# Kernel optimization log

Measured on AMD Instinct MI355X. Metric: run time of the kernel, lower is better.

Reference implementation:

```python
import jax, jax.numpy as jnp
import numpy as np

PE_SIZE = 16          # sqrt(num_patches=256)
HIDDEN_STRIDE = 2
CUBIC_A = -0.75       # torch bicubic coefficient


def cubic_resize_matrix(in_size, out_size, a=CUBIC_A):
    """(out_size, in_size) weights for torch bicubic, align_corners=False."""
    dst = np.arange(out_size)
    src = (dst + 0.5) * in_size / out_size - 0.5
    x0 = np.floor(src).astype(np.int64)
    W = np.zeros((out_size, in_size), np.float32)
    for k in range(-1, 3):  # 4 taps
        idx = np.clip(x0 + k, 0, in_size - 1)  # border replicate
        d = np.abs(src - (x0 + k))
        w = np.where(d <= 1.0, (a + 2) * d**3 - (a + 3) * d**2 + 1.0,
            np.where(d < 2.0, a * d**3 - 5 * a * d**2 + 8 * a * d - 4 * a, 0.0))
        np.add.at(W, (dst, idx), w.astype(np.float32))
    return W


def setup_inputs() -> dict:
    key = jax.random.key(0)
    k1, k2, k3, k4 = jax.random.split(key, 4)
    n_img, t, h, w = 8, 1, 64, 64
    total = n_img * t * h * w  # 32768 patches
    in_feat, d = 3 * 14 * 14, 1152
    return {
        "pixel_values": jax.random.normal(k1, (total, in_feat), jnp.float32),
        "w_patch": jax.random.normal(k2, (d, in_feat), jnp.float32) * 0.02,
        "b_patch": jax.random.normal(k3, (d,), jnp.float32) * 0.02,
        "pos_table": jax.random.normal(k4, (PE_SIZE * PE_SIZE, d), jnp.float32) * 0.02,
        "grid_thws": jnp.array([[t, h, w]] * n_img, jnp.int64),
    }


def _pos_embed(pos_table, grid):
    """grid: np int array (n_img, 3) -> (sum t*h*w, d) positional embeddings."""
    d = pos_table.shape[-1]
    pe_grid = pos_table.reshape(PE_SIZE, PE_SIZE, d)  # (H, W, d)
    s = HIDDEN_STRIDE
    pieces = []
    for t, h, w in grid:
        Wh = jnp.asarray(cubic_resize_matrix(PE_SIZE, int(h)))
        Ww = jnp.asarray(cubic_resize_matrix(PE_SIZE, int(w)))
        pe = jnp.einsum('hH,wW,HWd->hwd', Wh, Ww, pe_grid)  # (h, w, d)
        # hidden_stride window rearrange: (h,w,d) -> (h/s, w/s, s, s, d)
        pe = pe.reshape(h // s, s, w // s, s, d).transpose(0, 2, 1, 3, 4)
        pe = pe.reshape(h * w, d)
        pe = jnp.tile(pe, (int(t), 1))  # repeat over temporal dim
        pieces.append(pe)
    return jnp.concatenate(pieces, axis=0)


def reference(pixel_values, w_patch, b_patch, pos_table, grid_thws):
    # patch embedding (Linear)
    patch_embeds = pixel_values @ w_patch.T + b_patch  # (N, d)
    grid = np.asarray(grid_thws)  # static shapes per image
    pos = _pos_embed(pos_table, grid)
    return patch_embeds + pos
```

## Files before the change

### kernel.cpp

```cpp
#include <hip/hip_runtime.h>

typedef unsigned short ushort_t;
typedef unsigned int uint_t;

typedef __bf16 bf16x8 __attribute__((ext_vector_type(8)));
typedef float f32x4 __attribute__((ext_vector_type(4)));

#define KK 588
#define KP 608
#define NN 1152
#define MM 32768
#define POSROWS 4096
#define NSTEP 19
#define GRID 2304
#define CHUNKS_PER_ROW 76
#define BCHUNKS (NN * CHUNKS_PER_ROW)
#define BBLOCKS ((BCHUNKS + 255) / 256)


__device__ __forceinline__ void cubic_taps(int dst, float* w, int* idx) {
    const float A = -0.75f;
    float src = (float)dst * 0.25f - 0.25f;
    int x0 = (int)floorf(src);
    #pragma unroll
    for (int k = -1; k <= 2; ++k) {
        int i = x0 + k;
        int ic = i < 0 ? 0 : (i > 15 ? 15 : i);
        float d = fabsf(src - (float)i);
        float wt;
        if (d <= 1.0f)      wt = ((A + 2.0f) * d - (A + 3.0f)) * d * d + 1.0f;
        else if (d < 2.0f)  wt = ((A * d - 5.0f * A) * d + 8.0f * A) * d - 4.0f * A;
        else                wt = 0.0f;
        w[k + 1] = wt;
        idx[k + 1] = ic;
    }
}


__global__ void prep_kernel(const float* __restrict__ wp, ushort_t* __restrict__ wb,
                            const float* __restrict__ pt, const float* __restrict__ bias,
                            float* __restrict__ pos) {
    int b = blockIdx.x;
    if (b < BBLOCKS) {
        int c = b * 256 + threadIdx.x;
        if (c >= BCHUNKS) return;
        int row = c / CHUNKS_PER_ROW;
        int k0 = (c - row * CHUNKS_PER_ROW) * 8;
        const float* g = wp + (size_t)row * KK + k0;
        bf16x8 v;
        if (k0 + 8 <= KK) {
            f32x4 a = *(const f32x4*)g;
            f32x4 bb = *(const f32x4*)(g + 4);
            #pragma unroll
            for (int e = 0; e < 4; ++e) { v[e] = (__bf16)a[e]; v[e + 4] = (__bf16)bb[e]; }
        } else {
            #pragma unroll
            for (int e = 0; e < 8; ++e)
                v[e] = (k0 + e < KK) ? (__bf16)g[e] : (__bf16)0.f;
        }
        *(bf16x8*)(wb + (size_t)row * KP + k0) = v;
    } else {
        int n = b - BBLOCKS;
        int h = ((n >> 7) << 1) | ((n >> 1) & 1);
        int w = (((n >> 2) & 31) << 1) | (n & 1);
        float wh[4], ww[4];
        int ih[4], iw[4];
        cubic_taps(h, wh, ih);
        cubic_taps(w, ww, iw);
        const f32x4* pt4 = (const f32x4*)pt;
        const f32x4* bias4 = (const f32x4*)bias;
        for (int j = threadIdx.x; j < NN / 4; j += blockDim.x) {
            f32x4 s = bias4[j];
            #pragma unroll
            for (int a = 0; a < 4; ++a) {
                #pragma unroll
                for (int bq = 0; bq < 4; ++bq) {
                    float wt = wh[a] * ww[bq];
                    f32x4 vv = pt4[(ih[a] * 16 + iw[bq]) * (NN / 4) + j];
                    s.x += wt * vv.x; s.y += wt * vv.y; s.z += wt * vv.z; s.w += wt * vv.w;
                }
            }
            ((f32x4*)pos)[(size_t)n * (NN / 4) + j] = s;
        }
    }
}


__global__ __launch_bounds__(256, 3)
void gemm_kernel(const float* __restrict__ A,
                 const ushort_t* __restrict__ Bbf,
                 const float* __restrict__ pos,
                 float* __restrict__ out) {
    __shared__ __align__(16) ushort_t lA[2][128 * 32];
    __shared__ __align__(16) ushort_t lB[3][128 * 32];

    const int t = threadIdx.x;
    const int lane = t & 63;
    const int lm = lane & 15;
    const int lq = lane >> 4;
    const int wid = t >> 6;
    const int wm = wid >> 1, wn = wid & 1;

    const int arow = t >> 1;
    const int akh = (t & 1) * 16;
    const int asw = (arow >> 1) & 3;
    const int aq0 = (t & 1) * 2;

    int linear = (int)blockIdx.x;
    int xcd = linear & 7;
    int local = linear >> 3;
    int wg = xcd * (GRID / 8) + local;
    int mt = wg / 9;
    int nt = wg - mt * 9;
    const int bm = mt * 128;
    const int bn = nt * 128;

    f32x4 acc[4][4] = {};
    f32x4 rA0[4], rA1[4];

    auto loadA_fast = [&](int ks, f32x4* r) {
        const float* g = A + (size_t)(bm + arow) * KK + ks * 32 + akh;
        r[0] = *(const f32x4*)g;
        r[1] = *(const f32x4*)(g + 4);
        r[2] = *(const f32x4*)(g + 8);
        r[3] = *(const f32x4*)(g + 12);
    };
    auto loadA_guard = [&](int ks, f32x4* r) {
        const float* gr = A + (size_t)(bm + arow) * KK;
        int kb = ks * 32 + akh;
        #pragma unroll
        for (int e = 0; e < 16; ++e) {
            int k = kb + e;
            r[e >> 2][e & 3] = (k < KK) ? gr[k] : 0.f;
        }
    };
    auto cvtwrA = [&](int tile, const f32x4* r) {
        bf16x8 v0, v1;
        #pragma unroll
        for (int e = 0; e < 4; ++e) { v0[e] = (__bf16)r[0][e]; v0[e + 4] = (__bf16)r[1][e]; }
        #pragma unroll
        for (int e = 0; e < 4; ++e) { v1[e] = (__bf16)r[2][e]; v1[e + 4] = (__bf16)r[3][e]; }
        ushort_t* base = &lA[tile & 1][arow * 32];
        *(bf16x8*)(base + (aq0 ^ asw) * 8) = v0;
        *(bf16x8*)(base + ((aq0 + 1) ^ asw) * 8) = v1;
    };
    auto stageB = [&](int ks, int buf) {
        const int k0 = ks * 32;
        #pragma unroll
        for (int j = 0; j < 2; ++j) {
            int idx = j * 256 + t;
            int row = idx >> 2;
            int slot = idx & 3;
            int khi = slot ^ ((row >> 1) & 3);
            const ushort_t* gB = Bbf + (size_t)(bn + row) * KP + k0 + khi * 8;
            ushort_t* lBp = &lB[buf][(size_t)(idx & ~63) * 8];
            __builtin_amdgcn_global_load_lds(
                (const __attribute__((address_space(1))) void*)gB,
                (__attribute__((address_space(3))) void*)lBp, 16, 0, 0);
        }
    };

    auto step = [&](int ks, f32x4* rload, f32x4* rcvt) {
        const bool issue = (ks + 2 < NSTEP);
        if (issue) {
            if (ks + 2 == NSTEP - 1) loadA_guard(ks + 2, rload);
            else                     loadA_fast(ks + 2, rload);
            stageB(ks + 2, (ks + 2) % 3);
        }
        __builtin_amdgcn_sched_barrier(0);

        bf16x8 af[4], bfr[4];
        const ushort_t* bufA = lA[ks & 1];
        const ushort_t* bufB = lB[ks % 3];
        #pragma unroll
        for (int mi = 0; mi < 4; ++mi) {
            int row = wm * 64 + mi * 16 + lm;
            int slot = lq ^ ((row >> 1) & 3);
            af[mi] = *(const bf16x8*)(bufA + row * 32 + slot * 8);
        }
        #pragma unroll
        for (int ni = 0; ni < 4; ++ni) {
            int row = wn * 64 + ni * 16 + lm;
            int slot = lq ^ ((row >> 1) & 3);
            bfr[ni] = *(const bf16x8*)(bufB + row * 32 + slot * 8);
        }
        #pragma unroll
        for (int mi = 0; mi < 4; ++mi)
            #pragma unroll
            for (int ni = 0; ni < 4; ++ni)
                acc[mi][ni] = __builtin_amdgcn_mfma_f32_16x16x32_bf16(
                    bfr[ni], af[mi], acc[mi][ni], 0, 0, 0);

        if (issue) asm volatile("s_waitcnt vmcnt(6)" ::: "memory");
        else       asm volatile("s_waitcnt vmcnt(0)" ::: "memory");
        if (ks + 1 < NSTEP) cvtwrA(ks + 1, rcvt);
        asm volatile("s_waitcnt lgkmcnt(0)" ::: "memory");
        __builtin_amdgcn_s_barrier();
    };

    loadA_fast(0, rA0); stageB(0, 0);
    loadA_fast(1, rA1); stageB(1, 1);
    asm volatile("s_waitcnt vmcnt(6)" ::: "memory");
    cvtwrA(0, rA0);
    asm volatile("s_waitcnt lgkmcnt(0)" ::: "memory");
    __builtin_amdgcn_s_barrier();

    for (int ks = 0; ks < NSTEP - 2; ks += 2) {
        step(ks, rA0, rA1);
        step(ks + 1, rA1, rA0);
    }

    {
        bf16x8 af[4], bfr[4];
        const ushort_t* bufA = lA[0];
        const ushort_t* bufB = lB[0];
        #pragma unroll
        for (int mi = 0; mi < 4; ++mi) {
            int row = wm * 64 + mi * 16 + lm;
            int slot = lq ^ ((row >> 1) & 3);
            af[mi] = *(const bf16x8*)(bufA + row * 32 + slot * 8);
        }
        #pragma unroll
        for (int ni = 0; ni < 4; ++ni) {
            int row = wn * 64 + ni * 16 + lm;
            int slot = lq ^ ((row >> 1) & 3);
            bfr[ni] = *(const bf16x8*)(bufB + row * 32 + slot * 8);
        }
        #pragma unroll
        for (int mi = 0; mi < 4; ++mi)
            #pragma unroll
            for (int ni = 0; ni < 4; ++ni)
                acc[mi][ni] = __builtin_amdgcn_mfma_f32_16x16x32_bf16(
                    bfr[ni], af[mi], acc[mi][ni], 0, 0, 0);
    }

    const int M0 = bm + wm * 64;
    const int N0 = bn + wn * 64;
    #pragma unroll
    for (int mi = 0; mi < 4; ++mi) {
        int m = M0 + mi * 16 + lm;
        const float* posrow = pos + (size_t)(m & (POSROWS - 1)) * NN;
        float* outrow = out + (size_t)m * NN;
        #pragma unroll
        for (int ni = 0; ni < 4; ++ni) {
            int nb = N0 + ni * 16 + lq * 4;
            f32x4 p = *(const f32x4*)(posrow + nb);
            f32x4 v = acc[mi][ni];
            v.x += p.x; v.y += p.y; v.z += p.z; v.w += p.w;
            *(f32x4*)(outrow + nb) = v;
        }
    }
}


__global__ void fb_kernel(const float* __restrict__ A, const float* __restrict__ W,
                          const float* __restrict__ bias, const float* __restrict__ pt,
                          float* __restrict__ out) {
    __shared__ float sA[16][17], sB[16][17];
    int ty = threadIdx.y, tx = threadIdx.x;
    int row = blockIdx.y * 16 + ty;
    int col = blockIdx.x * 16 + tx;
    float acc = 0.f;
    for (int k0 = 0; k0 < KK; k0 += 16) {
        int ka = k0 + tx;
        sA[ty][tx] = (ka < KK) ? A[(size_t)row * KK + ka] : 0.f;
        sB[ty][tx] = (ka < KK) ? W[(size_t)(blockIdx.x * 16 + ty) * KK + ka] : 0.f;
        __syncthreads();
        #pragma unroll
        for (int kk = 0; kk < 16; ++kk)
            acc += sA[ty][kk] * sB[tx][kk];
        __syncthreads();
    }
    int n = row & (POSROWS - 1);
    int h = ((n >> 7) << 1) | ((n >> 1) & 1);
    int w = (((n >> 2) & 31) << 1) | (n & 1);
    float wh[4], ww[4]; int ih[4], iw[4];
    cubic_taps(h, wh, ih);
    cubic_taps(w, ww, iw);
    float p = 0.f;
    #pragma unroll
    for (int a = 0; a < 4; ++a) {
        float rs = 0.f;
        #pragma unroll
        for (int b = 0; b < 4; ++b)
            rs += ww[b] * pt[(ih[a] * 16 + iw[b]) * NN + col];
        p += wh[a] * rs;
    }
    out[(size_t)row * NN + col] = acc + bias[col] + p;
}


extern "C" void kernel_launch(void* const* d_in, const int* in_sizes, int n_in,
                              void* d_out, int out_size, void* d_ws, size_t ws_size,
                              hipStream_t stream) {
    const float* pv   = (const float*)d_in[0];
    const float* wp   = (const float*)d_in[1];
    const float* bias = (const float*)d_in[2];
    const float* pt   = (const float*)d_in[3];
    float* out = (float*)d_out;

    const size_t pos_bytes = (size_t)POSROWS * NN * 4;
    const size_t wb_bytes  = (size_t)NN * KP * 2;
    const size_t need = pos_bytes + wb_bytes;

    if (ws_size >= need) {
        float* pos = (float*)d_ws;
        ushort_t* wb = (ushort_t*)((char*)d_ws + pos_bytes);

        prep_kernel<<<BBLOCKS + POSROWS, 256, 0, stream>>>(wp, wb, pt, bias, pos);
        gemm_kernel<<<GRID, 256, 0, stream>>>(pv, wb, pos, out);
    } else {
        fb_kernel<<<dim3(NN / 16, MM / 16), dim3(16, 16), 0, stream>>>(pv, wp, bias, pt, out);
    }
}
```

Baseline: 140.2 us.

## Stage fp32 A tiles directly into LDS and convert to bf16 at fragment read

Replaces the register-staged A path (global load, convert to bf16, write LDS) with direct global-to-LDS async loads of fp32 A tiles. The conversion to bf16 now happens when MFMA fragments are read from LDS. The pipeline becomes a simple two-buffer prefetch loop for both A and B, with launch bounds relaxed and a new block-to-tile mapping across XCDs. This removes register pressure and the explicit convert-and-store step, but doubles A's LDS footprint, duplicates the conversion across waves that share A rows, and shortens the prefetch depth for B.

```diff
diff --git a/kernel.cpp b/kernel.cpp
--- a/kernel.cpp
+++ b/kernel.cpp
@@ -16,6 +16,9 @@
 #define CHUNKS_PER_ROW 76
 #define BCHUNKS (NN * CHUNKS_PER_ROW)
 #define BBLOCKS ((BCHUNKS + 255) / 256)
+
+#define AS1 __attribute__((address_space(1)))
+#define AS3 __attribute__((address_space(3)))
 
 
 __device__ __forceinline__ void cubic_taps(int dst, float* w, int* idx) {
@@ -86,13 +89,13 @@
 }
 
 
-__global__ __launch_bounds__(256, 3)
+__global__ __launch_bounds__(256)
 void gemm_kernel(const float* __restrict__ A,
                  const ushort_t* __restrict__ Bbf,
                  const float* __restrict__ pos,
                  float* __restrict__ out) {
-    __shared__ __align__(16) ushort_t lA[2][128 * 32];
-    __shared__ __align__(16) ushort_t lB[3][128 * 32];
+    __shared__ __align__(16) float    lA[2][128 * 32];
+    __shared__ __align__(16) ushort_t lB[2][128 * 32];
 
     const int t = threadIdx.x;
     const int lane = t & 63;
@@ -101,48 +104,34 @@
     const int wid = t >> 6;
     const int wm = wid >> 1, wn = wid & 1;
 
-    const int arow = t >> 1;
-    const int akh = (t & 1) * 16;
-    const int asw = (arow >> 1) & 3;
-    const int aq0 = (t & 1) * 2;
-
-    int linear = (int)blockIdx.x;
-    int xcd = linear & 7;
-    int local = linear >> 3;
-    int wg = xcd * (GRID / 8) + local;
-    int mt = wg / 9;
-    int nt = wg - mt * 9;
+    int blk = (int)blockIdx.x;
+    int xcd = blk & 7;
+    int local = blk >> 3;
+    int pp = local / 72;
+    int rem = local - pp * 72;
+    int nt = rem >> 3;
+    int r  = rem & 7;
+    int p  = pp * 8 + xcd;
+    int mt = r * 32 + p;
     const int bm = mt * 128;
     const int bn = nt * 128;
 
     f32x4 acc[4][4] = {};
-    f32x4 rA0[4], rA1[4];
-
-    auto loadA_fast = [&](int ks, f32x4* r) {
-        const float* g = A + (size_t)(bm + arow) * KK + ks * 32 + akh;
-        r[0] = *(const f32x4*)g;
-        r[1] = *(const f32x4*)(g + 4);
-        r[2] = *(const f32x4*)(g + 8);
-        r[3] = *(const f32x4*)(g + 12);
-    };
-    auto loadA_guard = [&](int ks, f32x4* r) {
-        const float* gr = A + (size_t)(bm + arow) * KK;
-        int kb = ks * 32 + akh;
-        #pragma unroll
-        for (int e = 0; e < 16; ++e) {
-            int k = kb + e;
-            r[e >> 2][e & 3] = (k < KK) ? gr[k] : 0.f;
-        }
-    };
-    auto cvtwrA = [&](int tile, const f32x4* r) {
-        bf16x8 v0, v1;
-        #pragma unroll
-        for (int e = 0; e < 4; ++e) { v0[e] = (__bf16)r[0][e]; v0[e + 4] = (__bf16)r[1][e]; }
-        #pragma unroll
-        for (int e = 0; e < 4; ++e) { v1[e] = (__bf16)r[2][e]; v1[e + 4] = (__bf16)r[3][e]; }
-        ushort_t* base = &lA[tile & 1][arow * 32];
-        *(bf16x8*)(base + (aq0 ^ asw) * 8) = v0;
-        *(bf16x8*)(base + ((aq0 + 1) ^ asw) * 8) = v1;
+
+    auto stageA = [&](int ks, int buf) {
+        const int k0 = ks * 32;
+        #pragma unroll
+        for (int j = 0; j < 4; ++j) {
+            int idx = j * 256 + t;
+            int row = idx >> 3;
+            int slot = idx & 7;
+            int sc = slot ^ (row & 7);
+            int kf = k0 + sc * 4;
+            const float* g = A + (size_t)(bm + row) * KK + ((kf <= KK - 4) ? kf : 0);
+            float* lp = &lA[buf][(idx & ~63) * 4];
+            __builtin_amdgcn_global_load_lds(
+                (const AS1 void*)g, (AS3 void*)lp, 16, 0, 0);
+        }
     };
     auto stageB = [&](int ks, int buf) {
         const int k0 = ks * 32;
@@ -155,34 +144,43 @@
             const ushort_t* gB = Bbf + (size_t)(bn + row) * KP + k0 + khi * 8;
             ushort_t* lBp = &lB[buf][(size_t)(idx & ~63) * 8];
             __builtin_amdgcn_global_load_lds(
-                (const __attribute__((address_space(1))) void*)gB,
-                (__attribute__((address_space(3))) void*)lBp, 16, 0, 0);
+                (const AS1 void*)gB, (AS3 void*)lBp, 16, 0, 0);
         }
     };
 
-    auto step = [&](int ks, f32x4* rload, f32x4* rcvt) {
-        const bool issue = (ks + 2 < NSTEP);
-        if (issue) {
-            if (ks + 2 == NSTEP - 1) loadA_guard(ks + 2, rload);
-            else                     loadA_fast(ks + 2, rload);
-            stageB(ks + 2, (ks + 2) % 3);
-        }
+    stageA(0, 0); stageB(0, 0);
+
+    for (int ks = 0; ks < NSTEP; ++ks) {
+        const int cur = ks & 1;
+        if (ks + 1 < NSTEP) {
+            stageA(ks + 1, cur ^ 1);
+            stageB(ks + 1, cur ^ 1);
+            asm volatile("s_waitcnt vmcnt(6)" ::: "memory");
+        } else {
+            asm volatile("s_waitcnt vmcnt(0)" ::: "memory");
+        }
+        __builtin_amdgcn_s_barrier();
         __builtin_amdgcn_sched_barrier(0);
 
         bf16x8 af[4], bfr[4];
-        const ushort_t* bufA = lA[ks & 1];
-        const ushort_t* bufB = lB[ks % 3];
         #pragma unroll
         for (int mi = 0; mi < 4; ++mi) {
             int row = wm * 64 + mi * 16 + lm;
-            int slot = lq ^ ((row >> 1) & 3);
-            af[mi] = *(const bf16x8*)(bufA + row * 32 + slot * 8);
+            int s0 = (2 * lq) ^ (row & 7);
+            const float* base = &lA[cur][row * 32];
+            f32x4 v0 = *(const f32x4*)(base + s0 * 4);
+            f32x4 v1 = *(const f32x4*)(base + (s0 ^ 1) * 4);
+            #pragma unroll
+            for (int e = 0; e < 4; ++e) {
+                af[mi][e]     = (__bf16)v0[e];
+                af[mi][e + 4] = (__bf16)v1[e];
+            }
         }
         #pragma unroll
         for (int ni = 0; ni < 4; ++ni) {
             int row = wn * 64 + ni * 16 + lm;
             int slot = lq ^ ((row >> 1) & 3);
-            bfr[ni] = *(const bf16x8*)(bufB + row * 32 + slot * 8);
+            bfr[ni] = *(const bf16x8*)(&lB[cur][row * 32 + slot * 8]);
         }
         #pragma unroll
         for (int mi = 0; mi < 4; ++mi)
@@ -191,47 +189,9 @@
                 acc[mi][ni] = __builtin_amdgcn_mfma_f32_16x16x32_bf16(
                     bfr[ni], af[mi], acc[mi][ni], 0, 0, 0);
 
-        if (issue) asm volatile("s_waitcnt vmcnt(6)" ::: "memory");
-        else       asm volatile("s_waitcnt vmcnt(0)" ::: "memory");
-        if (ks + 1 < NSTEP) cvtwrA(ks + 1, rcvt);
         asm volatile("s_waitcnt lgkmcnt(0)" ::: "memory");
+        __builtin_amdgcn_sched_barrier(0);
         __builtin_amdgcn_s_barrier();
-    };
-
-    loadA_fast(0, rA0); stageB(0, 0);
-    loadA_fast(1, rA1); stageB(1, 1);
-    asm volatile("s_waitcnt vmcnt(6)" ::: "memory");
-    cvtwrA(0, rA0);
-    asm volatile("s_waitcnt lgkmcnt(0)" ::: "memory");
-    __builtin_amdgcn_s_barrier();
-
-    for (int ks = 0; ks < NSTEP - 2; ks += 2) {
-        step(ks, rA0, rA1);
-        step(ks + 1, rA1, rA0);
-    }
-
-    {
-        bf16x8 af[4], bfr[4];
-        const ushort_t* bufA = lA[0];
-        const ushort_t* bufB = lB[0];
-        #pragma unroll
-        for (int mi = 0; mi < 4; ++mi) {
-            int row = wm * 64 + mi * 16 + lm;
-            int slot = lq ^ ((row >> 1) & 3);
-            af[mi] = *(const bf16x8*)(bufA + row * 32 + slot * 8);
-        }
-        #pragma unroll
-        for (int ni = 0; ni < 4; ++ni) {
-            int row = wn * 64 + ni * 16 + lm;
-            int slot = lq ^ ((row >> 1) & 3);
-            bfr[ni] = *(const bf16x8*)(bufB + row * 32 + slot * 8);
-        }
-        #pragma unroll
-        for (int mi = 0; mi < 4; ++mi)
-            #pragma unroll
-            for (int ni = 0; ni < 4; ++ni)
-                acc[mi][ni] = __builtin_amdgcn_mfma_f32_16x16x32_bf16(
-                    bfr[ni], af[mi], acc[mi][ni], 0, 0, 0);
     }
 
     const int M0 = bm + wm * 64;
@@ -244,9 +204,9 @@
         #pragma unroll
         for (int ni = 0; ni < 4; ++ni) {
             int nb = N0 + ni * 16 + lq * 4;
-            f32x4 p = *(const f32x4*)(posrow + nb);
+            f32x4 pv = *(const f32x4*)(posrow + nb);
             f32x4 v = acc[mi][ni];
-            v.x += p.x; v.y += p.y; v.z += p.z; v.w += p.w;
+            v.x += pv.x; v.y += pv.y; v.z += pv.z; v.w += pv.w;
             *(f32x4*)(outrow + nb) = v;
         }
     }
@@ -277,16 +237,16 @@
     float wh[4], ww[4]; int ih[4], iw[4];
     cubic_taps(h, wh, ih);
     cubic_taps(w, ww, iw);
-    float p = 0.f;
+    float pq = 0.f;
     #pragma unroll
     for (int a = 0; a < 4; ++a) {
         float rs = 0.f;
         #pragma unroll
         for (int b = 0; b < 4; ++b)
             rs += ww[b] * pt[(ih[a] * 16 + iw[b]) * NN + col];
-        p += wh[a] * rs;
-    }
-    out[(size_t)row * NN + col] = acc + bias[col] + p;
+        pq += wh[a] * rs;
+    }
+    out[(size_t)row * NN + col] = acc + bias[col] + pq;
 }
 
 
```

Result: slower. 163.4 us (+16.5%).
